# Kernel optimization log

Hardware: AMD Instinct MI355X
Metric: run time of the kernel (lower is better)

The kernel has to match this reference:

```python
import jax, jax.numpy as jnp
import numpy as np

B, T, C = 2, 2048, 2048
NH, NKV = 16, 4
HD = C // NH  # 128


def setup_inputs() -> dict:
    key = jax.random.key(0)
    ks = jax.random.split(key, 5)
    w = lambda k, shape: jax.random.normal(k, shape, jnp.float32) * 0.02
    return {
        "x": jax.random.normal(ks[0], (B, T, C), jnp.float32),
        "Wq": w(ks[1], (C, C)),
        "Wk": w(ks[2], (C, NKV * HD)),
        "Wv": w(ks[3], (C, NKV * HD)),
        "Wproj": w(ks[4], (C, C)),
    }


def _rope(x):
    # x: [B, H, T, D]; rotate-half RoPE with base 10000
    D = x.shape[-1]
    t = x.shape[-2]
    inv_freq = 1.0 / (10000.0 ** (jnp.arange(0, D, 2, dtype=jnp.float32) / D))
    freqs = jnp.arange(t, dtype=jnp.float32)[:, None] * inv_freq[None, :]  # [T, D/2]
    emb = jnp.concatenate([freqs, freqs], axis=-1)  # [T, D]
    cos, sin = jnp.cos(emb), jnp.sin(emb)
    x1, x2 = x[..., : D // 2], x[..., D // 2 :]
    rotated = jnp.concatenate([-x2, x1], axis=-1)
    return x * cos + rotated * sin


def reference(x, Wq, Wk, Wv, Wproj):
    b, t, c = x.shape
    q = (x @ Wq).reshape(b, t, NH, HD).transpose(0, 2, 1, 3)    # [B,NH,T,HD]
    k = (x @ Wk).reshape(b, t, NKV, HD).transpose(0, 2, 1, 3)   # [B,NKV,T,HD]
    v = (x @ Wv).reshape(b, t, NKV, HD).transpose(0, 2, 1, 3)
    q = _rope(q)
    k = _rope(k)
    rep = NH // NKV
    k = jnp.repeat(k, rep, axis=1)  # [B,NH,T,HD]
    v = jnp.repeat(v, rep, axis=1)
    scale = 1.0 / jnp.sqrt(jnp.float32(HD))
    scores = jnp.einsum("bhqd,bhkd->bhqk", q, k) * scale        # [B,NH,T,T]
    causal = jnp.tril(jnp.ones((t, t), dtype=bool))
    scores = jnp.where(causal, scores, jnp.finfo(scores.dtype).min)
    attn = jax.nn.softmax(scores, axis=-1)
    y = jnp.einsum("bhqk,bhkd->bhqd", attn, v)                  # [B,NH,T,HD]
    y = y.transpose(0, 2, 1, 3).reshape(b, t, c)
    return y @ Wproj
```

## Files before the change

### kernel.cpp

```cpp
#include <hip/hip_runtime.h>

#define B_ 2
#define T_ 2048
#define C_ 2048
#define NH_ 16
#define NKV_ 4
#define HD_ 128
#define M_ 4096
#define NQKV_ 3072

typedef __bf16 bf16x8 __attribute__((ext_vector_type(8)));
typedef float f32x4 __attribute__((ext_vector_type(4)));
typedef float f32x16 __attribute__((ext_vector_type(16)));

__device__ __forceinline__ unsigned short f2bf(float f) {
  union { float f; unsigned u; } c{f};
  unsigned u = c.u + 0x7FFFu + ((c.u >> 16) & 1u);
  return (unsigned short)(u >> 16);
}
__device__ __forceinline__ float bf2f(unsigned short h) {
  union { unsigned u; float f; } c{(unsigned)h << 16};
  return c.f;
}

#define GLOAD_LDS16(g, l)                                        \
  __builtin_amdgcn_global_load_lds(                              \
      (const __attribute__((address_space(1))) void*)(g),        \
      (__attribute__((address_space(3))) void*)(l), 16, 0, 0)

__global__ void rope_table_kernel(float2* __restrict__ rt) {
  int t = blockIdx.x, i = threadIdx.x;
  float inv = powf(10000.f, -(float)(2 * i) / 128.f);
  float s, c;
  sincosf((float)t * inv, &s, &c);
  rt[t * 64 + i] = make_float2(c, s);
}

__global__ void convx_kernel(const float* __restrict__ x, unsigned short* __restrict__ xb, int n4) {
  int i = blockIdx.x * blockDim.x + threadIdx.x;
  if (i >= n4) return;
  float4 v = reinterpret_cast<const float4*>(x)[i];
  union { ushort4 u; unsigned short s[4]; } o;
  o.s[0] = f2bf(v.x); o.s[1] = f2bf(v.y); o.s[2] = f2bf(v.z); o.s[3] = f2bf(v.w);
  reinterpret_cast<ushort4*>(xb)[i] = o.u;
}

__global__ void transpose_conv4_kernel(const float* __restrict__ Wq, const float* __restrict__ Wk,
                                       const float* __restrict__ Wv, const float* __restrict__ Wp,
                                       unsigned short* __restrict__ wt) {
  __shared__ float tile[32][33];
  int id = blockIdx.x;
  const float* W;
  unsigned short* Wt;
  int N, bx, by;
  if (id < 4096)      { W = Wq; Wt = wt;                          N = 2048; int u = id;        bx = u & 63; by = u >> 6; }
  else if (id < 5120) { W = Wk; Wt = wt + (size_t)2048 * 2048;    N = 512;  int u = id - 4096; bx = u & 15; by = u >> 4; }
  else if (id < 6144) { W = Wv; Wt = wt + (size_t)2560 * 2048;    N = 512;  int u = id - 5120; bx = u & 15; by = u >> 4; }
  else                { W = Wp; Wt = wt + (size_t)3072 * 2048;    N = 2048; int u = id - 6144; bx = u & 63; by = u >> 6; }
  const int K = 2048;
  bx *= 32; by *= 32;
  int tx = threadIdx.x & 31, ty = threadIdx.x >> 5;
#pragma unroll
  for (int r = 0; r < 32; r += 8)
    tile[ty + r][tx] = W[(size_t)(by + ty + r) * N + bx + tx];
  __syncthreads();
#pragma unroll
  for (int r = 0; r < 32; r += 8)
    Wt[(size_t)(bx + ty + r) * K + by + tx] = f2bf(tile[tx][ty + r]);
}

__global__ void transpose_v_kernel(const unsigned short* __restrict__ qkv,
                                   unsigned short* __restrict__ vt) {
  __shared__ unsigned short tile[32][33];
  int bh = blockIdx.z;
  int b = bh >> 2, kvh = bh & 3;
  int t0 = blockIdx.x * 32, d0 = blockIdx.y * 32;
  int tx = threadIdx.x & 31, ty = threadIdx.x >> 5;
#pragma unroll
  for (int r = 0; r < 32; r += 8)
    tile[ty + r][tx] = qkv[(size_t)(b * T_ + t0 + ty + r) * NQKV_ + 2560 + kvh * HD_ + d0 + tx];
  __syncthreads();
#pragma unroll
  for (int r = 0; r < 32; r += 8)
    vt[(size_t)(bh * HD_ + d0 + ty + r) * T_ + t0 + tx] = tile[tx][ty + r];
}

template <typename OUT, bool ROPE>
__global__ __launch_bounds__(256) void gemm_bf16(const unsigned short* __restrict__ A,
                                                 const unsigned short* __restrict__ Bt,
                                                 OUT* __restrict__ Cm,
                                                 const float2* __restrict__ rt,
                                                 int M, int N, int K) {
  constexpr int BK = 32;
  __shared__ __align__(16) unsigned short Al[2][128 * BK];
  __shared__ __align__(16) unsigned short Bl[2][128 * BK];
  int tid = threadIdx.x, w = tid >> 6, lane = tid & 63;
  int l15 = lane & 15, l4 = lane >> 4;
  size_t arow0 = (size_t)blockIdx.y * 128;
  size_t brow0 = (size_t)blockIdx.x * 128;

  f32x4 acc[2][8];
#pragma unroll
  for (int mi = 0; mi < 2; ++mi)
#pragma unroll
    for (int ni = 0; ni < 8; ++ni) acc[mi][ni] = (f32x4){0.f, 0.f, 0.f, 0.f};

  auto stage = [&](int buf, int k0) {
#pragma unroll
    for (int i = 0; i < 2; ++i) {
      int c = i * 256 + w * 64 + lane;
      const unsigned short* g = A + (arow0 + (c >> 2)) * K + k0 + (c & 3) * 8;
      GLOAD_LDS16(g, &Al[buf][(i * 4 + w) * 512]);
    }
#pragma unroll
    for (int i = 0; i < 2; ++i) {
      int c = i * 256 + w * 64 + lane;
      const unsigned short* g = Bt + (brow0 + (c >> 2)) * K + k0 + (c & 3) * 8;
      GLOAD_LDS16(g, &Bl[buf][(i * 4 + w) * 512]);
    }
  };

  stage(0, 0);
  __syncthreads();
  int NT = K / BK, cur = 0;
  for (int kt = 0; kt < NT; ++kt) {
    if (kt + 1 < NT) stage(cur ^ 1, (kt + 1) * BK);
    const unsigned short* Ab = &Al[cur][0];
    const unsigned short* Bb = &Bl[cur][0];
    bf16x8 af[2], bfr[8];
#pragma unroll
    for (int mi = 0; mi < 2; ++mi)
      af[mi] = *reinterpret_cast<const bf16x8*>(Ab + (w * 32 + mi * 16 + l15) * BK + l4 * 8);
#pragma unroll
    for (int ni = 0; ni < 8; ++ni)
      bfr[ni] = *reinterpret_cast<const bf16x8*>(Bb + (ni * 16 + l15) * BK + l4 * 8);
#pragma unroll
    for (int mi = 0; mi < 2; ++mi)
#pragma unroll
      for (int ni = 0; ni < 8; ++ni)
        acc[mi][ni] = __builtin_amdgcn_mfma_f32_16x16x32_bf16(af[mi], bfr[ni], acc[mi][ni], 0, 0, 0);
    __syncthreads();
    cur ^= 1;
  }

  bool dorope = ROPE && (brow0 < 2560);
#pragma unroll
  for (int mi = 0; mi < 2; ++mi)
#pragma unroll
    for (int r = 0; r < 4; ++r) {
      size_t row = arow0 + w * 32 + mi * 16 + l4 * 4 + r;
      if (dorope) {
        int t = (int)(row & (T_ - 1));
#pragma unroll
        for (int ni = 0; ni < 4; ++ni) {
          float2 cs = rt[t * 64 + ni * 16 + l15];
          float a1 = acc[mi][ni][r], a2 = acc[mi][ni + 4][r];
          size_t col = brow0 + ni * 16 + l15;
          Cm[row * N + col]      = f2bf(a1 * cs.x - a2 * cs.y);
          Cm[row * N + col + 64] = f2bf(a2 * cs.x + a1 * cs.y);
        }
      } else {
#pragma unroll
        for (int ni = 0; ni < 8; ++ni) {
          size_t col = brow0 + ni * 16 + l15;
          float v = acc[mi][ni][r];
          if constexpr (sizeof(OUT) == 4) Cm[row * N + col] = v;
          else                            Cm[row * N + col] = f2bf(v);
        }
      }
    }
}

__global__ __launch_bounds__(256, 2) void attn_kernel(const unsigned short* __restrict__ qkv,
                                                      const unsigned short* __restrict__ vt,
                                                      unsigned short* __restrict__ att) {
  constexpr int KB = 64;
  __shared__ __align__(16) unsigned short Kl[2][KB * 128];
  __shared__ __align__(16) unsigned short Vl[2][128 * KB];
  int tid = threadIdx.x, w = tid >> 6, lane = tid & 63;
  int l31 = lane & 31, hi = lane >> 5;
  int h4 = hi * 4;

  int id = blockIdx.x;
  int u = id & 255, half = id >> 8;
  int bh = u & 31;
  int qh = u >> 5;
  int qi = half ? (15 - qh) : qh;
  int q0 = qi * 128;
  int b = bh >> 4, hd = bh & 15, kvh = hd >> 2;
  int qr0 = q0 + w * 32;
  int ql = qr0 + l31;

  bf16x8 qf[8];
  {
    const unsigned short* qb = qkv + (size_t)(b * T_ + ql) * NQKV_ + hd * HD_ + hi * 8;
    const float scale = 0.08838834764831845f * 1.4426950408889634f;
#pragma unroll
    for (int df = 0; df < 8; ++df) {
      bf16x8 t = *reinterpret_cast<const bf16x8*>(qb + df * 16);
#pragma unroll
      for (int j = 0; j < 8; ++j) t[j] = (__bf16)((float)t[j] * scale);
      qf[df] = t;
    }
  }

  f32x16 o[4];
#pragma unroll
  for (int dt = 0; dt < 4; ++dt)
#pragma unroll
    for (int r = 0; r < 16; ++r) o[dt][r] = 0.f;
  float mr = -1e30f, lr = 0.f;

  auto stage = [&](int buf, int kv0) {
#pragma unroll
    for (int i = 0; i < 4; ++i) {
      int c = (i * 4 + w) * 64 + lane;
      int g = c ^ ((c >> 4) & 7);
      const unsigned short* src =
          qkv + (size_t)(b * T_ + kv0 + (g >> 4)) * NQKV_ + C_ + kvh * HD_ + (g & 15) * 8;
      GLOAD_LDS16(src, &Kl[buf][(i * 4 + w) * 512]);
    }
#pragma unroll
    for (int i = 0; i < 4; ++i) {
      int c = (i * 4 + w) * 64 + lane;
      int g = c ^ ((c >> 3) & 7);
      const unsigned short* src =
          vt + (size_t)((b * NKV_ + kvh) * HD_ + (g >> 3)) * T_ + kv0 + (g & 7) * 8;
      GLOAD_LDS16(src, &Vl[buf][(i * 4 + w) * 512]);
    }
  };

  int nt = q0 / KB + 2;
  stage(0, 0);
  __syncthreads();
  int cur = 0;
  for (int kt = 0; kt < nt; ++kt) {
    int kv0 = kt * KB;
    if (kt + 1 < nt) stage(cur ^ 1, kv0 + KB);

    if (kv0 <= qr0 + 31) {
      f32x16 s[2];
#pragma unroll
      for (int r = 0; r < 16; ++r) { s[0][r] = 0.f; s[1][r] = 0.f; }
      const unsigned short* Kb = &Kl[cur][0];
      __builtin_amdgcn_s_setprio(1);
#pragma unroll
      for (int t2 = 0; t2 < 2; ++t2)
#pragma unroll
        for (int df = 0; df < 8; ++df) {
          bf16x8 kf = *reinterpret_cast<const bf16x8*>(
              Kb + (((t2 * 32 + l31) * 128 + df * 16 + hi * 8) ^ ((l31 & 7) << 3)));
          s[t2] = __builtin_amdgcn_mfma_f32_32x32x16_bf16(kf, qf[df], s[t2], 0, 0, 0);
        }
      __builtin_amdgcn_s_setprio(0);

      float rm = -1e30f;
      if ((kv0 + KB - 1) > qr0) {
#pragma unroll
        for (int t2 = 0; t2 < 2; ++t2)
#pragma unroll
          for (int r = 0; r < 16; ++r) {
            float sv = s[t2][r];
            int kcol = kv0 + t2 * 32 + (r & 3) + 8 * (r >> 2) + h4;
            if (kcol > ql) sv = -1e30f;
            s[t2][r] = sv;
            rm = fmaxf(rm, sv);
          }
      } else {
#pragma unroll
        for (int t2 = 0; t2 < 2; ++t2)
#pragma unroll
          for (int r = 0; r < 16; ++r) rm = fmaxf(rm, s[t2][r]);
      }
      rm = fmaxf(rm, __shfl_xor(rm, 32));

      if (!__all(rm <= mr + 11.0f)) {
        float mnew = fmaxf(mr, rm);
        float alpha = exp2f(mr - mnew);
        mr = mnew;
        lr *= alpha;
#pragma unroll
        for (int dt = 0; dt < 4; ++dt)
#pragma unroll
          for (int r = 0; r < 16; ++r) o[dt][r] *= alpha;
      }

      float ps = 0.f;
#pragma unroll
      for (int t2 = 0; t2 < 2; ++t2)
#pragma unroll
        for (int r = 0; r < 16; ++r) {
          float p = exp2f(s[t2][r] - mr);
          s[t2][r] = p;
          ps += p;
        }
      lr += ps;

      unsigned pk[2][8];
#pragma unroll
      for (int t2 = 0; t2 < 2; ++t2)
#pragma unroll
        for (int i = 0; i < 8; ++i) {
          union { unsigned u32; __bf16 hh[2]; } pr;
          pr.hh[0] = (__bf16)s[t2][2 * i];
          pr.hh[1] = (__bf16)s[t2][2 * i + 1];
          pk[t2][i] = pr.u32;
        }

      bf16x8 pb[4];
#pragma unroll
      for (int f = 0; f < 4; ++f) {
        int t2 = f >> 1, bq = (f & 1) * 4;
        union { bf16x8 v; unsigned d[4]; } fr;
#pragma unroll
        for (int p = 0; p < 2; ++p) {
          unsigned uu = pk[t2][bq + p];
          unsigned ww = pk[t2][bq + 2 + p];
          unsigned us = (unsigned)__shfl_xor((int)uu, 32);
          unsigned ws = (unsigned)__shfl_xor((int)ww, 32);
          fr.d[p]     = hi ? ws : uu;
          fr.d[2 + p] = hi ? ww : us;
        }
        pb[f] = fr.v;
      }

      const unsigned short* Vb = &Vl[cur][0];
      __builtin_amdgcn_s_setprio(1);
#pragma unroll
      for (int dt = 0; dt < 4; ++dt)
#pragma unroll
        for (int kf = 0; kf < 4; ++kf) {
          bf16x8 vf = *reinterpret_cast<const bf16x8*>(
              Vb + (((dt * 32 + l31) * KB + kf * 16 + hi * 8) ^ ((l31 & 7) << 3)));
          o[dt] = __builtin_amdgcn_mfma_f32_32x32x16_bf16(vf, pb[kf], o[dt], 0, 0, 0);
        }
      __builtin_amdgcn_s_setprio(0);
    }

    __syncthreads();
    cur ^= 1;
  }

  float ls = lr + __shfl_xor(lr, 32);
  float inv = 1.f / ls;
  unsigned short* ob = att + (size_t)(b * T_ + ql) * C_ + hd * HD_;
#pragma unroll
  for (int dt = 0; dt < 4; ++dt)
#pragma unroll
    for (int r = 0; r < 16; ++r) {
      int d = dt * 32 + (r & 3) + 8 * (r >> 2) + h4;
      ob[d] = f2bf(o[dt][r] * inv);
    }
}

extern "C" void kernel_launch(void* const* d_in, const int* in_sizes, int n_in,
                              void* d_out, int out_size, void* d_ws, size_t ws_size,
                              hipStream_t stream) {
  const float* x  = (const float*)d_in[0];
  const float* Wq = (const float*)d_in[1];
  const float* Wk = (const float*)d_in[2];
  const float* Wv = (const float*)d_in[3];
  const float* Wp = (const float*)d_in[4];
  float* out = (float*)d_out;
  char* ws = (char*)d_ws;

  unsigned short* xb  = (unsigned short*)(ws);
  unsigned short* wt  = (unsigned short*)(ws + 16777216);
  unsigned short* qkv = (unsigned short*)(ws + 37748736);
  float2*         rt  = (float2*)(ws + 62914560);
  unsigned short* vt  = (unsigned short*)(ws + 63963136);
  unsigned short* att = xb;

  rope_table_kernel<<<T_, 64, 0, stream>>>(rt);
  convx_kernel<<<(M_ * C_ / 4 + 255) / 256, 256, 0, stream>>>(x, xb, M_ * C_ / 4);
  transpose_conv4_kernel<<<dim3(10240), 256, 0, stream>>>(Wq, Wk, Wv, Wp, wt);

  gemm_bf16<unsigned short, true><<<dim3(NQKV_ / 128, M_ / 128), 256, 0, stream>>>(
      xb, wt, qkv, rt, M_, NQKV_, C_);
  transpose_v_kernel<<<dim3(T_ / 32, HD_ / 32, B_ * NKV_), 256, 0, stream>>>(qkv, vt);
  attn_kernel<<<dim3(512), 256, 0, stream>>>(qkv, vt, att);
  gemm_bf16<float, false><<<dim3(C_ / 128, M_ / 128), 256, 0, stream>>>(
      att, wt + (size_t)3072 * 2048, out, nullptr, M_, C_, C_);
}
```

Measured before the change: 220.2 us.

## Stage V through registers into a single LDS buffer to raise attention occupancy

The attention kernel keeps K double-buffered in LDS through direct global-to-LDS loads. V is now prefetched into registers and written into a single LDS buffer between the QK/softmax phase and the PV phase, with explicit vmcnt/lgkmcnt waits and split barriers. This cuts LDS use so launch bounds can be raised from 2 to 3 blocks per SIMD. The cross-half P shuffle is also replaced by v_permlane32_swap. The cost is extra VGPRs for V staging, a second barrier per tile, hand-tuned waitcnt counts that must stay exact, and one redundant K/V load on the final iteration.

```diff
diff --git a/kernel.cpp b/kernel.cpp
--- a/kernel.cpp
+++ b/kernel.cpp
@@ -171,12 +171,12 @@
     }
 }
 
-__global__ __launch_bounds__(256, 2) void attn_kernel(const unsigned short* __restrict__ qkv,
+__global__ __launch_bounds__(256, 3) void attn_kernel(const unsigned short* __restrict__ qkv,
                                                       const unsigned short* __restrict__ vt,
                                                       unsigned short* __restrict__ att) {
   constexpr int KB = 64;
   __shared__ __align__(16) unsigned short Kl[2][KB * 128];
-  __shared__ __align__(16) unsigned short Vl[2][128 * KB];
+  __shared__ __align__(16) unsigned short Vl[128 * KB];
   int tid = threadIdx.x, w = tid >> 6, lane = tid & 63;
   int l31 = lane & 31, hi = lane >> 5;
   int h4 = hi * 4;
@@ -211,7 +211,10 @@
     for (int r = 0; r < 16; ++r) o[dt][r] = 0.f;
   float mr = -1e30f, lr = 0.f;
 
-  auto stage = [&](int buf, int kv0) {
+  int nt = q0 / KB + 2;
+
+  auto stage_K = [&](int buf, int tile) {
+    int kv0 = tile * KB;
 #pragma unroll
     for (int i = 0; i < 4; ++i) {
       int c = (i * 4 + w) * 64 + lane;
@@ -220,29 +223,46 @@
           qkv + (size_t)(b * T_ + kv0 + (g >> 4)) * NQKV_ + C_ + kvh * HD_ + (g & 15) * 8;
       GLOAD_LDS16(src, &Kl[buf][(i * 4 + w) * 512]);
     }
+  };
+
+  uint4 vreg[4];
+  const unsigned short* vbase = vt + (size_t)((b * NKV_ + kvh) * HD_) * T_;
+  auto load_V = [&](int tile) {
+    int kv0 = tile * KB;
 #pragma unroll
     for (int i = 0; i < 4; ++i) {
-      int c = (i * 4 + w) * 64 + lane;
-      int g = c ^ ((c >> 3) & 7);
-      const unsigned short* src =
-          vt + (size_t)((b * NKV_ + kvh) * HD_ + (g >> 3)) * T_ + kv0 + (g & 7) * 8;
-      GLOAD_LDS16(src, &Vl[buf][(i * 4 + w) * 512]);
+      int d = w * 32 + i * 8 + (lane >> 3);
+      vreg[i] = *reinterpret_cast<const uint4*>(vbase + (size_t)d * T_ + kv0 + (lane & 7) * 8);
     }
   };
-
-  int nt = q0 / KB + 2;
-  stage(0, 0);
-  __syncthreads();
-  int cur = 0;
+  auto write_V = [&]() {
+#pragma unroll
+    for (int i = 0; i < 4; ++i) {
+      int d = w * 32 + i * 8 + (lane >> 3);
+      int kv8 = lane & 7;
+      *reinterpret_cast<uint4*>(&Vl[d * 64 + ((kv8 ^ (d & 7)) << 3)]) = vreg[i];
+    }
+  };
+
+  stage_K(0, 0);
+  load_V(0);
+
   for (int kt = 0; kt < nt; ++kt) {
     int kv0 = kt * KB;
-    if (kt + 1 < nt) stage(cur ^ 1, kv0 + KB);
-
-    if (kv0 <= qr0 + 31) {
+    int tnext = kt + 1 < nt ? kt + 1 : nt - 1;
+    stage_K((kt + 1) & 1, tnext);
+
+    asm volatile("s_waitcnt vmcnt(8)" ::: "memory");
+    __builtin_amdgcn_s_barrier();
+    __builtin_amdgcn_sched_barrier(0);
+
+    bool active = (kv0 <= qr0 + 31);
+    unsigned pk[2][8];
+    if (active) {
       f32x16 s[2];
 #pragma unroll
       for (int r = 0; r < 16; ++r) { s[0][r] = 0.f; s[1][r] = 0.f; }
-      const unsigned short* Kb = &Kl[cur][0];
+      const unsigned short* Kb = &Kl[kt & 1][0];
       __builtin_amdgcn_s_setprio(1);
 #pragma unroll
       for (int t2 = 0; t2 < 2; ++t2)
@@ -296,7 +316,6 @@
         }
       lr += ps;
 
-      unsigned pk[2][8];
 #pragma unroll
       for (int t2 = 0; t2 < 2; ++t2)
 #pragma unroll
@@ -306,7 +325,16 @@
           pr.hh[1] = (__bf16)s[t2][2 * i + 1];
           pk[t2][i] = pr.u32;
         }
-
+    }
+
+    asm volatile("s_waitcnt vmcnt(4)" ::: "memory");
+    write_V();
+    load_V(tnext);
+    asm volatile("s_waitcnt lgkmcnt(0)" ::: "memory");
+    __builtin_amdgcn_s_barrier();
+    __builtin_amdgcn_sched_barrier(0);
+
+    if (active) {
       bf16x8 pb[4];
 #pragma unroll
       for (int f = 0; f < 4; ++f) {
@@ -314,31 +342,26 @@
         union { bf16x8 v; unsigned d[4]; } fr;
 #pragma unroll
         for (int p = 0; p < 2; ++p) {
-          unsigned uu = pk[t2][bq + p];
-          unsigned ww = pk[t2][bq + 2 + p];
-          unsigned us = (unsigned)__shfl_xor((int)uu, 32);
-          unsigned ws = (unsigned)__shfl_xor((int)ww, 32);
-          fr.d[p]     = hi ? ws : uu;
-          fr.d[2 + p] = hi ? ww : us;
+          unsigned a = pk[t2][bq + p];
+          unsigned bb = pk[t2][bq + 2 + p];
+          asm("v_permlane32_swap_b32 %0, %1" : "+v"(a), "+v"(bb));
+          fr.d[p] = a;
+          fr.d[2 + p] = bb;
         }
         pb[f] = fr.v;
       }
 
-      const unsigned short* Vb = &Vl[cur][0];
       __builtin_amdgcn_s_setprio(1);
 #pragma unroll
       for (int dt = 0; dt < 4; ++dt)
 #pragma unroll
         for (int kf = 0; kf < 4; ++kf) {
           bf16x8 vf = *reinterpret_cast<const bf16x8*>(
-              Vb + (((dt * 32 + l31) * KB + kf * 16 + hi * 8) ^ ((l31 & 7) << 3)));
+              Vl + (((dt * 32 + l31) * KB + kf * 16 + hi * 8) ^ ((l31 & 7) << 3)));
           o[dt] = __builtin_amdgcn_mfma_f32_32x32x16_bf16(vf, pb[kf], o[dt], 0, 0, 0);
         }
       __builtin_amdgcn_s_setprio(0);
     }
-
-    __syncthreads();
-    cur ^= 1;
   }
 
   float ls = lr + __shfl_xor(lr, 32);
```

Result: slower. 369.5 us (+67.8%).

## Pre-pack V into MFMA fragment layout and load directly from global

Applied to the files above, without the earlier changes.

The V transpose kernel now writes V in a packed fragment-major layout (8 keys by 128 dims per chunk), so the attention kernel can load V operands straight from global memory into registers instead of staging them through LDS. The V LDS double buffer is removed, which frees shared memory. The register-level P repacking now uses v_permlane32_swap instead of shuffles plus selects. The risk is that V loads now come from global/L2 memory inside the inner loop, with only partial software prefetching, rather than being asynchronously staged ahead of use.

```diff
diff --git a/kernel.cpp b/kernel.cpp
--- a/kernel.cpp
+++ b/kernel.cpp
@@ -70,19 +70,30 @@
 }
 
 __global__ void transpose_v_kernel(const unsigned short* __restrict__ qkv,
-                                   unsigned short* __restrict__ vt) {
-  __shared__ unsigned short tile[32][33];
-  int bh = blockIdx.z;
+                                   unsigned short* __restrict__ vt2) {
+  __shared__ unsigned short tile[64][136];
+  int bt = blockIdx.x;
+  int bh = bt >> 5, t = bt & 31;
   int b = bh >> 2, kvh = bh & 3;
-  int t0 = blockIdx.x * 32, d0 = blockIdx.y * 32;
-  int tx = threadIdx.x & 31, ty = threadIdx.x >> 5;
-#pragma unroll
-  for (int r = 0; r < 32; r += 8)
-    tile[ty + r][tx] = qkv[(size_t)(b * T_ + t0 + ty + r) * NQKV_ + 2560 + kvh * HD_ + d0 + tx];
+  int tid = threadIdx.x;
+#pragma unroll
+  for (int p = 0; p < 4; ++p) {
+    int kv = p * 16 + (tid >> 4);
+    int c8 = (tid & 15) * 8;
+    *reinterpret_cast<uint4*>(&tile[kv][c8]) = *reinterpret_cast<const uint4*>(
+        &qkv[(size_t)(b * T_ + t * 64 + kv) * NQKV_ + 2560 + kvh * HD_ + c8]);
+  }
   __syncthreads();
 #pragma unroll
-  for (int r = 0; r < 32; r += 8)
-    vt[(size_t)(bh * HD_ + d0 + ty + r) * T_ + t0 + tx] = tile[tx][ty + r];
+  for (int it = 0; it < 4; ++it) {
+    int item = it * 256 + tid;
+    int pk = item >> 7, d = item & 127;
+    unsigned short tmp[8];
+#pragma unroll
+    for (int j = 0; j < 8; ++j) tmp[j] = tile[pk * 8 + j][d];
+    *reinterpret_cast<uint4*>(&vt2[((size_t)(bt * 8 + pk) * 128 + d) * 8]) =
+        *reinterpret_cast<uint4*>(tmp);
+  }
 }
 
 template <typename OUT, bool ROPE>
@@ -172,11 +183,10 @@
 }
 
 __global__ __launch_bounds__(256, 2) void attn_kernel(const unsigned short* __restrict__ qkv,
-                                                      const unsigned short* __restrict__ vt,
+                                                      const unsigned short* __restrict__ vt2,
                                                       unsigned short* __restrict__ att) {
   constexpr int KB = 64;
   __shared__ __align__(16) unsigned short Kl[2][KB * 128];
-  __shared__ __align__(16) unsigned short Vl[2][128 * KB];
   int tid = threadIdx.x, w = tid >> 6, lane = tid & 63;
   int l31 = lane & 31, hi = lane >> 5;
   int h4 = hi * 4;
@@ -211,7 +221,7 @@
     for (int r = 0; r < 16; ++r) o[dt][r] = 0.f;
   float mr = -1e30f, lr = 0.f;
 
-  auto stage = [&](int buf, int kv0) {
+  auto stage_K = [&](int buf, int kv0) {
 #pragma unroll
     for (int i = 0; i < 4; ++i) {
       int c = (i * 4 + w) * 64 + lane;
@@ -220,23 +230,17 @@
           qkv + (size_t)(b * T_ + kv0 + (g >> 4)) * NQKV_ + C_ + kvh * HD_ + (g & 15) * 8;
       GLOAD_LDS16(src, &Kl[buf][(i * 4 + w) * 512]);
     }
-#pragma unroll
-    for (int i = 0; i < 4; ++i) {
-      int c = (i * 4 + w) * 64 + lane;
-      int g = c ^ ((c >> 3) & 7);
-      const unsigned short* src =
-          vt + (size_t)((b * NKV_ + kvh) * HD_ + (g >> 3)) * T_ + kv0 + (g & 7) * 8;
-      GLOAD_LDS16(src, &Vl[buf][(i * 4 + w) * 512]);
-    }
   };
 
+  const unsigned short* vhead = vt2 + (size_t)((b * NKV_ + kvh) * 32) * 8192;
+
   int nt = q0 / KB + 2;
-  stage(0, 0);
+  stage_K(0, 0);
   __syncthreads();
   int cur = 0;
   for (int kt = 0; kt < nt; ++kt) {
     int kv0 = kt * KB;
-    if (kt + 1 < nt) stage(cur ^ 1, kv0 + KB);
+    if (kt + 1 < nt) stage_K(cur ^ 1, kv0 + KB);
 
     if (kv0 <= qr0 + 31) {
       f32x16 s[2];
@@ -307,6 +311,15 @@
           pk[t2][i] = pr.u32;
         }
 
+      const unsigned short* vb2 = vhead + (size_t)kt * 8192;
+      uint4 va[4], vc[4];
+#pragma unroll
+      for (int kf = 0; kf < 4; ++kf)
+        va[kf] = *reinterpret_cast<const uint4*>(vb2 + ((kf * 2 + hi) * 128 + l31) * 8);
+#pragma unroll
+      for (int kf = 0; kf < 4; ++kf)
+        vc[kf] = *reinterpret_cast<const uint4*>(vb2 + ((kf * 2 + hi) * 128 + 32 + l31) * 8);
+
       bf16x8 pb[4];
 #pragma unroll
       for (int f = 0; f < 4; ++f) {
@@ -314,26 +327,43 @@
         union { bf16x8 v; unsigned d[4]; } fr;
 #pragma unroll
         for (int p = 0; p < 2; ++p) {
-          unsigned uu = pk[t2][bq + p];
-          unsigned ww = pk[t2][bq + 2 + p];
-          unsigned us = (unsigned)__shfl_xor((int)uu, 32);
-          unsigned ws = (unsigned)__shfl_xor((int)ww, 32);
-          fr.d[p]     = hi ? ws : uu;
-          fr.d[2 + p] = hi ? ww : us;
+          unsigned a = pk[t2][bq + p];
+          unsigned bb = pk[t2][bq + 2 + p];
+          asm("v_permlane32_swap_b32 %0, %1" : "+v"(a), "+v"(bb));
+          fr.d[p] = a;
+          fr.d[2 + p] = bb;
         }
         pb[f] = fr.v;
       }
 
-      const unsigned short* Vb = &Vl[cur][0];
+      union Vc { uint4 u; bf16x8 v; };
       __builtin_amdgcn_s_setprio(1);
 #pragma unroll
-      for (int dt = 0; dt < 4; ++dt)
-#pragma unroll
-        for (int kf = 0; kf < 4; ++kf) {
-          bf16x8 vf = *reinterpret_cast<const bf16x8*>(
-              Vb + (((dt * 32 + l31) * KB + kf * 16 + hi * 8) ^ ((l31 & 7) << 3)));
-          o[dt] = __builtin_amdgcn_mfma_f32_32x32x16_bf16(vf, pb[kf], o[dt], 0, 0, 0);
-        }
+      for (int kf = 0; kf < 4; ++kf) {
+        Vc cv; cv.u = va[kf];
+        o[0] = __builtin_amdgcn_mfma_f32_32x32x16_bf16(cv.v, pb[kf], o[0], 0, 0, 0);
+      }
+#pragma unroll
+      for (int kf = 0; kf < 4; ++kf)
+        va[kf] = *reinterpret_cast<const uint4*>(vb2 + ((kf * 2 + hi) * 128 + 64 + l31) * 8);
+#pragma unroll
+      for (int kf = 0; kf < 4; ++kf) {
+        Vc cv; cv.u = vc[kf];
+        o[1] = __builtin_amdgcn_mfma_f32_32x32x16_bf16(cv.v, pb[kf], o[1], 0, 0, 0);
+      }
+#pragma unroll
+      for (int kf = 0; kf < 4; ++kf)
+        vc[kf] = *reinterpret_cast<const uint4*>(vb2 + ((kf * 2 + hi) * 128 + 96 + l31) * 8);
+#pragma unroll
+      for (int kf = 0; kf < 4; ++kf) {
+        Vc cv; cv.u = va[kf];
+        o[2] = __builtin_amdgcn_mfma_f32_32x32x16_bf16(cv.v, pb[kf], o[2], 0, 0, 0);
+      }
+#pragma unroll
+      for (int kf = 0; kf < 4; ++kf) {
+        Vc cv; cv.u = vc[kf];
+        o[3] = __builtin_amdgcn_mfma_f32_32x32x16_bf16(cv.v, pb[kf], o[3], 0, 0, 0);
+      }
       __builtin_amdgcn_s_setprio(0);
     }
 
@@ -377,7 +407,7 @@
 
   gemm_bf16<unsigned short, true><<<dim3(NQKV_ / 128, M_ / 128), 256, 0, stream>>>(
       xb, wt, qkv, rt, M_, NQKV_, C_);
-  transpose_v_kernel<<<dim3(T_ / 32, HD_ / 32, B_ * NKV_), 256, 0, stream>>>(qkv, vt);
+  transpose_v_kernel<<<dim3(256), 256, 0, stream>>>(qkv, vt);
   attn_kernel<<<dim3(512), 256, 0, stream>>>(qkv, vt, att);
   gemm_bf16<float, false><<<dim3(C_ / 128, M_ / 128), 256, 0, stream>>>(
       att, wt + (size_t)3072 * 2048, out, nullptr, M_, C_, C_);
```

New measurement: 222.5 us. Within noise of the previous version (+1.0%).

## Replace GEMMs with 8-wave ping-pong pipelined kernel using larger tiles and swizzled LDS

Applied to the files above, without the earlier changes.

Both bf16 GEMMs now run in a new 512-thread kernel with 256x256 (QKV) or 128x256 (proj) tiles and four LDS slots. The kernel interleaves global-to-LDS prefetches of the next K tiles between MFMA phases, using explicit vmcnt waits, barriers and s_setprio. It also XOR-swizzles the LDS layout to avoid bank conflicts. The aim is to hide memory latency and raise MFMA utilisation. The cost is much more LDS and registers per block (one block per CU) and fewer blocks for the projection GEMM, which may underfill the GPU.

```diff
diff --git a/kernel.cpp b/kernel.cpp
--- a/kernel.cpp
+++ b/kernel.cpp
@@ -17,10 +17,6 @@
   union { float f; unsigned u; } c{f};
   unsigned u = c.u + 0x7FFFu + ((c.u >> 16) & 1u);
   return (unsigned short)(u >> 16);
-}
-__device__ __forceinline__ float bf2f(unsigned short h) {
-  union { unsigned u; float f; } c{(unsigned)h << 16};
-  return c.f;
 }
 
 #define GLOAD_LDS16(g, l)                                        \
@@ -85,85 +81,135 @@
     vt[(size_t)(bh * HD_ + d0 + ty + r) * T_ + t0 + tx] = tile[tx][ty + r];
 }
 
-template <typename OUT, bool ROPE>
-__global__ __launch_bounds__(256) void gemm_bf16(const unsigned short* __restrict__ A,
+template <int BM, typename OUT, bool ROPE>
+__global__ __launch_bounds__(512, 1) void gemm8p(const unsigned short* __restrict__ A,
                                                  const unsigned short* __restrict__ Bt,
                                                  OUT* __restrict__ Cm,
                                                  const float2* __restrict__ rt,
                                                  int M, int N, int K) {
-  constexpr int BK = 32;
-  __shared__ __align__(16) unsigned short Al[2][128 * BK];
-  __shared__ __align__(16) unsigned short Bl[2][128 * BK];
-  int tid = threadIdx.x, w = tid >> 6, lane = tid & 63;
+  constexpr int MR = BM / 64;
+  __shared__ __align__(16) unsigned short As[2][2][BM * 32];
+  __shared__ __align__(16) unsigned short Bs[2][2][256 * 32];
+  int tid = threadIdx.x, wid = tid >> 6, lane = tid & 63;
   int l15 = lane & 15, l4 = lane >> 4;
-  size_t arow0 = (size_t)blockIdx.y * 128;
-  size_t brow0 = (size_t)blockIdx.x * 128;
-
-  f32x4 acc[2][8];
-#pragma unroll
-  for (int mi = 0; mi < 2; ++mi)
-#pragma unroll
-    for (int ni = 0; ni < 8; ++ni) acc[mi][ni] = (f32x4){0.f, 0.f, 0.f, 0.f};
-
-  auto stage = [&](int buf, int k0) {
+  int wr = wid >> 1, wc = wid & 1;
+  size_t arow0 = (size_t)blockIdx.y * BM;
+  size_t brow0 = (size_t)blockIdx.x * 256;
+  int tmax = K / 64 - 1;
+
+  f32x4 acc[MR][8];
+#pragma unroll
+  for (int m = 0; m < MR; ++m)
+#pragma unroll
+    for (int n = 0; n < 8; ++n) acc[m][n] = (f32x4){0.f, 0.f, 0.f, 0.f};
+
+  auto stageA = [&](int slot, int kh, int tile) {
+    int k0 = tile * 64 + kh * 32;
+    constexpr int NLD = (BM * 32 * 2) / (512 * 16);
+#pragma unroll
+    for (int i = 0; i < NLD; ++i) {
+      int c = i * 512 + wid * 64 + lane;
+      int rg = c >> 2, cg = (c & 3) ^ (rg & 3);
+      const unsigned short* g = A + (arow0 + rg) * K + k0 + cg * 8;
+      GLOAD_LDS16(g, &As[slot][kh][c * 8]);
+    }
+  };
+  auto stageB = [&](int slot, int kh, int tile) {
+    int k0 = tile * 64 + kh * 32;
 #pragma unroll
     for (int i = 0; i < 2; ++i) {
-      int c = i * 256 + w * 64 + lane;
-      const unsigned short* g = A + (arow0 + (c >> 2)) * K + k0 + (c & 3) * 8;
-      GLOAD_LDS16(g, &Al[buf][(i * 4 + w) * 512]);
-    }
-#pragma unroll
-    for (int i = 0; i < 2; ++i) {
-      int c = i * 256 + w * 64 + lane;
-      const unsigned short* g = Bt + (brow0 + (c >> 2)) * K + k0 + (c & 3) * 8;
-      GLOAD_LDS16(g, &Bl[buf][(i * 4 + w) * 512]);
+      int c = i * 512 + wid * 64 + lane;
+      int rg = c >> 2, cg = (c & 3) ^ (rg & 3);
+      const unsigned short* g = Bt + (brow0 + rg) * K + k0 + cg * 8;
+      GLOAD_LDS16(g, &Bs[slot][kh][c * 8]);
     }
   };
 
-  stage(0, 0);
-  __syncthreads();
-  int NT = K / BK, cur = 0;
-  for (int kt = 0; kt < NT; ++kt) {
-    if (kt + 1 < NT) stage(cur ^ 1, (kt + 1) * BK);
-    const unsigned short* Ab = &Al[cur][0];
-    const unsigned short* Bb = &Bl[cur][0];
-    bf16x8 af[2], bfr[8];
-#pragma unroll
-    for (int mi = 0; mi < 2; ++mi)
-      af[mi] = *reinterpret_cast<const bf16x8*>(Ab + (w * 32 + mi * 16 + l15) * BK + l4 * 8);
-#pragma unroll
-    for (int ni = 0; ni < 8; ++ni)
-      bfr[ni] = *reinterpret_cast<const bf16x8*>(Bb + (ni * 16 + l15) * BK + l4 * 8);
-#pragma unroll
-    for (int mi = 0; mi < 2; ++mi)
-#pragma unroll
-      for (int ni = 0; ni < 8; ++ni)
-        acc[mi][ni] = __builtin_amdgcn_mfma_f32_16x16x32_bf16(af[mi], bfr[ni], acc[mi][ni], 0, 0, 0);
-    __syncthreads();
-    cur ^= 1;
+  stageA(0, 0, 0); stageB(0, 0, 0); stageA(0, 1, 0); stageB(0, 1, 0);
+  stageA(1, 0, 1); stageB(1, 0, 1); stageA(1, 1, 1);
+  if constexpr (BM == 256) asm volatile("s_waitcnt vmcnt(6)" ::: "memory");
+  else                     asm volatile("s_waitcnt vmcnt(4)" ::: "memory");
+  __builtin_amdgcn_s_barrier();
+  __builtin_amdgcn_sched_barrier(0);
+
+  int NT2 = K / 128;
+  for (int it = 0; it < NT2; ++it) {
+    int t2 = it * 2;
+#pragma unroll
+    for (int tt = 0; tt < 2; ++tt) {
+      bf16x8 af[MR];
+#pragma unroll
+      for (int kh = 0; kh < 2; ++kh) {
+#pragma unroll
+        for (int nh = 0; nh < 2; ++nh) {
+          int p = tt * 4 + kh * 2 + nh + 1;
+          if (nh == 0) {
+#pragma unroll
+            for (int m = 0; m < MR; ++m) {
+              int r = wr * (MR * 16) + m * 16 + l15;
+              af[m] = *reinterpret_cast<const bf16x8*>(
+                  &As[tt][kh][r * 32 + ((l4 ^ (r & 3)) * 8)]);
+            }
+          }
+          bf16x8 bf[4];
+#pragma unroll
+          for (int j = 0; j < 4; ++j) {
+            int r = wc * 128 + (nh * 4 + j) * 16 + l15;
+            bf[j] = *reinterpret_cast<const bf16x8*>(
+                &Bs[tt][kh][r * 32 + ((l4 ^ (r & 3)) * 8)]);
+          }
+          if (p == 1) stageB(1, 1, t2 + 1);
+          if (p == 2) stageA(0, 0, t2 + 2 <= tmax ? t2 + 2 : tmax);
+          if (p == 3) stageB(0, 0, t2 + 2 <= tmax ? t2 + 2 : tmax);
+          if (p == 4) stageA(0, 1, t2 + 2 <= tmax ? t2 + 2 : tmax);
+          if (p == 5) stageB(0, 1, t2 + 2 <= tmax ? t2 + 2 : tmax);
+          if (p == 6) stageA(1, 0, t2 + 3 <= tmax ? t2 + 3 : tmax);
+          if (p == 7) stageB(1, 0, t2 + 3 <= tmax ? t2 + 3 : tmax);
+          if (p == 8) stageA(1, 1, t2 + 3 <= tmax ? t2 + 3 : tmax);
+
+          __builtin_amdgcn_s_barrier();
+          asm volatile("s_waitcnt lgkmcnt(0)" ::: "memory");
+          __builtin_amdgcn_sched_barrier(0);
+          __builtin_amdgcn_s_setprio(1);
+#pragma unroll
+          for (int m = 0; m < MR; ++m)
+#pragma unroll
+            for (int j = 0; j < 4; ++j)
+              acc[m][nh * 4 + j] = __builtin_amdgcn_mfma_f32_16x16x32_bf16(
+                  af[m], bf[j], acc[m][nh * 4 + j], 0, 0, 0);
+          __builtin_amdgcn_s_setprio(0);
+          if (p == 4 || p == 8) {
+            if constexpr (BM == 256) asm volatile("s_waitcnt vmcnt(6)" ::: "memory");
+            else                     asm volatile("s_waitcnt vmcnt(4)" ::: "memory");
+          }
+          __builtin_amdgcn_s_barrier();
+          __builtin_amdgcn_sched_barrier(0);
+        }
+      }
+    }
   }
 
-  bool dorope = ROPE && (brow0 < 2560);
-#pragma unroll
-  for (int mi = 0; mi < 2; ++mi)
+  bool dorope = ROPE && (brow0 + wc * 128 < 2560);
+#pragma unroll
+  for (int m = 0; m < MR; ++m)
 #pragma unroll
     for (int r = 0; r < 4; ++r) {
-      size_t row = arow0 + w * 32 + mi * 16 + l4 * 4 + r;
+      size_t row = arow0 + wr * (MR * 16) + m * 16 + l4 * 4 + r;
       if (dorope) {
         int t = (int)(row & (T_ - 1));
 #pragma unroll
-        for (int ni = 0; ni < 4; ++ni) {
-          float2 cs = rt[t * 64 + ni * 16 + l15];
-          float a1 = acc[mi][ni][r], a2 = acc[mi][ni + 4][r];
-          size_t col = brow0 + ni * 16 + l15;
+        for (int n = 0; n < 4; ++n) {
+          float2 cs = rt[t * 64 + n * 16 + l15];
+          float a1 = acc[m][n][r], a2 = acc[m][n + 4][r];
+          size_t col = brow0 + wc * 128 + n * 16 + l15;
           Cm[row * N + col]      = f2bf(a1 * cs.x - a2 * cs.y);
           Cm[row * N + col + 64] = f2bf(a2 * cs.x + a1 * cs.y);
         }
       } else {
 #pragma unroll
-        for (int ni = 0; ni < 8; ++ni) {
-          size_t col = brow0 + ni * 16 + l15;
-          float v = acc[mi][ni][r];
+        for (int n = 0; n < 8; ++n) {
+          size_t col = brow0 + wc * 128 + n * 16 + l15;
+          float v = acc[m][n][r];
           if constexpr (sizeof(OUT) == 4) Cm[row * N + col] = v;
           else                            Cm[row * N + col] = f2bf(v);
         }
@@ -375,10 +421,10 @@
   convx_kernel<<<(M_ * C_ / 4 + 255) / 256, 256, 0, stream>>>(x, xb, M_ * C_ / 4);
   transpose_conv4_kernel<<<dim3(10240), 256, 0, stream>>>(Wq, Wk, Wv, Wp, wt);
 
-  gemm_bf16<unsigned short, true><<<dim3(NQKV_ / 128, M_ / 128), 256, 0, stream>>>(
+  gemm8p<256, unsigned short, true><<<dim3(NQKV_ / 256, M_ / 256), 512, 0, stream>>>(
       xb, wt, qkv, rt, M_, NQKV_, C_);
   transpose_v_kernel<<<dim3(T_ / 32, HD_ / 32, B_ * NKV_), 256, 0, stream>>>(qkv, vt);
   attn_kernel<<<dim3(512), 256, 0, stream>>>(qkv, vt, att);
-  gemm_bf16<float, false><<<dim3(C_ / 128, M_ / 128), 256, 0, stream>>>(
+  gemm8p<128, float, false><<<dim3(C_ / 256, M_ / 128), 512, 0, stream>>>(
       att, wt + (size_t)3072 * 2048, out, nullptr, M_, C_, C_);
 }
```

Result: slower. 233.7 us (+6.1%).
